# Performance work log

Hardware: AMD Instinct MI355X
Metric: run time of the kernel (lower is better)

Reference implementation:

```python
import jax, jax.numpy as jnp
import numpy as np

CHEB_K = 3
EMBED_DIM = 16
N_NODES = 2048
DIM = 64


def setup_inputs() -> dict:
    key = jax.random.key(0)
    k1, k2, k3, k4 = jax.random.split(key, 4)
    B, N, T, D = 16, N_NODES, 12, DIM
    x = jax.random.normal(k1, (B, N, T, D), dtype=jnp.float32)
    node_embeddings = jax.random.normal(k2, (N, EMBED_DIM), dtype=jnp.float32)
    # xavier-uniform-ish init for pools
    wp_bound = float(np.sqrt(6.0 / (EMBED_DIM * CHEB_K * D + D)))
    weights_pool = jax.random.uniform(k3, (EMBED_DIM, CHEB_K, D, D), dtype=jnp.float32,
                                      minval=-wp_bound, maxval=wp_bound)
    bias_pool = jax.random.uniform(k4, (EMBED_DIM, D), dtype=jnp.float32)
    return {"x": x, "node_embeddings": node_embeddings,
            "weights_pool": weights_pool, "bias_pool": bias_pool}


def reference(x, node_embeddings, weights_pool, bias_pool):
    B, N, T, D = x.shape
    cheb_k = weights_pool.shape[1]
    # [B,N,T,D] -> [B*T, N, D]
    xr = jnp.transpose(x, (0, 2, 1, 3)).reshape(B * T, N, D)
    # adaptive adjacency: row-softmax of relu gram matrix  [N,N]
    supports = jax.nn.softmax(jax.nn.relu(node_embeddings @ node_embeddings.T), axis=1)
    # Chebyshev polynomial basis of the adaptive support
    support_set = [jnp.eye(N, dtype=supports.dtype), supports]
    for _ in range(2, cheb_k):
        support_set.append(2.0 * supports @ support_set[-1] - support_set[-2])
    supports_k = jnp.stack(support_set, axis=0)  # [K,N,N]
    # hypernetwork: per-node weights/bias from embeddings
    weights = jnp.einsum('nd,dkio->nkio', node_embeddings, weights_pool)  # [N,K,D,D]
    bias = node_embeddings @ bias_pool  # [N,D]
    # graph conv: gather K-hop aggregates, then per-node grouped GEMM
    x_g = jnp.einsum('knm,bmc->bnkc', supports_k, xr)  # [B*T,N,K,D]
    x_gconv = jnp.einsum('bnki,nkio->bno', x_g, weights) + bias  # [B*T,N,D]
    return jnp.transpose(x_gconv.reshape(B, T, N, D), (0, 2, 1, 3))
```

## Files before the change

kernel.cpp:

```cpp
#include <hip/hip_runtime.h>
#include <hip/hip_bf16.h>

#define N_NODES 2048
#define EMB 16
#define NT 12
#define BT 192
#define C_COLS 12288
#define TD 768
#define BSTRIDE (N_NODES * TD)
#define KDIM 2048

typedef unsigned short u16;
typedef unsigned int u32;
typedef __attribute__((ext_vector_type(8))) __bf16 bf16x8;
typedef __attribute__((ext_vector_type(8))) u16 u16x8;
typedef __attribute__((ext_vector_type(4))) float f32x4;

__device__ __forceinline__ u16 f2bfu(float f) {
    u32 u = __float_as_uint(f);
    return (u16)((u + 0x7FFFu + ((u >> 16) & 1u)) >> 16);
}
__device__ __forceinline__ float bfu2f(u16 h) {
    return __uint_as_float(((u32)h) << 16);
}

__device__ __forceinline__ void gl2lds16(const void* g, void* l) {
    __builtin_amdgcn_global_load_lds(
        (const __attribute__((address_space(1))) u32*)g,
        (__attribute__((address_space(3))) u32*)l, 16, 0, 0);
}

__global__ void supports_kernel(const float* __restrict__ E, u16* __restrict__ Sb)
{
    __shared__ float en[EMB];
    __shared__ float red[256];
    const int n = blockIdx.x;
    const int tid = threadIdx.x;
    if (tid < EMB) en[tid] = E[n * EMB + tid];
    __syncthreads();

    float v[8];
    float mx = 0.0f;
    #pragma unroll
    for (int j = 0; j < 8; ++j) {
        const int m = tid + j * 256;
        const float* em = E + m * EMB;
        float acc = 0.f;
        #pragma unroll
        for (int d = 0; d < EMB; ++d) acc += en[d] * em[d];
        acc = fmaxf(acc, 0.f);
        v[j] = acc;
        mx = fmaxf(mx, acc);
    }
    red[tid] = mx;
    __syncthreads();
    for (int s = 128; s > 0; s >>= 1) {
        if (tid < s) red[tid] = fmaxf(red[tid], red[tid + s]);
        __syncthreads();
    }
    mx = red[0];
    __syncthreads();

    float sum = 0.f;
    #pragma unroll
    for (int j = 0; j < 8; ++j) { v[j] = __expf(v[j] - mx); sum += v[j]; }
    red[tid] = sum;
    __syncthreads();
    for (int s = 128; s > 0; s >>= 1) {
        if (tid < s) red[tid] += red[tid + s];
        __syncthreads();
    }
    const float inv = 1.f / red[0];
    #pragma unroll
    for (int j = 0; j < 8; ++j)
        Sb[(size_t)n * KDIM + tid + j * 256] = f2bfu(v[j] * inv);
}

__global__ void xcast_kernel(const float* __restrict__ x, u16* __restrict__ XbT, int c0g)
{
    __shared__ u16 tile[64][65];
    const int tid = threadIdx.x;
    const int cg = c0g + blockIdx.x * 64;
    const int b = cg / TD;
    const int r0 = cg - b * TD;
    const int m0 = blockIdx.y * 64;
    const float* xp = x + (size_t)b * BSTRIDE + (size_t)m0 * TD + r0;

    const int lc = tid & 63;
    const int rg = tid >> 6;
    #pragma unroll
    for (int j = 0; j < 16; ++j) {
        const int mr = j * 4 + rg;
        tile[lc][mr] = f2bfu(xp[(size_t)mr * TD + lc]);
    }
    __syncthreads();
    u16* op = XbT + (size_t)(blockIdx.x * 64) * KDIM + m0;
    #pragma unroll
    for (int j = 0; j < 16; ++j) {
        const int cr = j * 4 + rg;
        op[(size_t)cr * KDIM + lc] = tile[cr][lc];
    }
}

template <int MODE>
__launch_bounds__(256, 3)
__global__ void mfma_gemm(const u16* __restrict__ A,
                          const u16* __restrict__ B,
                          u16* __restrict__ OutT,
                          u16* __restrict__ OutRow,
                          const u16* __restrict__ Xc,
                          int c0g)
{
    __shared__ char smem[16384];
    char* As = smem;
    char* Bs = smem + 8192;

    const int tid = threadIdx.x;
    const int lane = tid & 63;
    const int w = tid >> 6;
    const int wm = w >> 1, wn = w & 1;
    const int ln15 = lane & 15, quad = lane >> 4;

    const int m0 = blockIdx.y * 128;
    const int cb = blockIdx.x * 128;

    const int q0 = 2 * w, q1 = 2 * w + 1;
    const int srow = lane >> 2;
    const int skol = (lane & 3) * 8;
    const u16* ga0 = A + (size_t)(m0 + q0 * 16 + srow) * KDIM + skol;
    const u16* ga1 = A + (size_t)(m0 + q1 * 16 + srow) * KDIM + skol;
    const u16* gb0 = B + (size_t)(cb + q0 * 16 + srow) * KDIM + skol;
    const u16* gb1 = B + (size_t)(cb + q1 * 16 + srow) * KDIM + skol;
    char* la0 = As + q0 * 1024;
    char* la1 = As + q1 * 1024;
    char* lb0 = Bs + q0 * 1024;
    char* lb1 = Bs + q1 * 1024;

    f32x4 acc[4][4] = {};

    for (int k0 = 0; k0 < KDIM; k0 += 32) {
        __syncthreads();
        gl2lds16(ga0, la0);
        gl2lds16(ga1, la1);
        gl2lds16(gb0, lb0);
        gl2lds16(gb1, lb1);
        ga0 += 32; ga1 += 32; gb0 += 32; gb1 += 32;
        __syncthreads();

        bf16x8 af[4], bg[4];
        #pragma unroll
        for (int i = 0; i < 4; ++i) {
            af[i] = *(const bf16x8*)(As + ((wm * 64 + i * 16 + ln15) * 64 + quad * 16));
            bg[i] = *(const bf16x8*)(Bs + ((wn * 64 + i * 16 + ln15) * 64 + quad * 16));
        }
        #pragma unroll
        for (int mi = 0; mi < 4; ++mi)
            #pragma unroll
            for (int ni = 0; ni < 4; ++ni)
                acc[mi][ni] = __builtin_amdgcn_mfma_f32_16x16x32_bf16(
                    af[mi], bg[ni], acc[mi][ni], 0, 0, 0);
    }

    const int mbase = m0 + wm * 64 + quad * 4;
    const int cbase = cb + wn * 64 + ln15;
    #pragma unroll
    for (int mi = 0; mi < 4; ++mi) {
        #pragma unroll
        for (int ni = 0; ni < 4; ++ni) {
            const f32x4 v = acc[mi][ni];
            const int mm = mbase + mi * 16;
            const int cc = cbase + ni * 16;
            if (MODE == 0) {
                ushort4 u;
                u.x = f2bfu(v.x); u.y = f2bfu(v.y); u.z = f2bfu(v.z); u.w = f2bfu(v.w);
                *(ushort4*)(OutT + (size_t)cc * KDIM + mm) = u;
                u16* orow = OutRow + (size_t)mm * C_COLS + c0g + cc;
                orow[0 * C_COLS] = u.x;
                orow[1 * C_COLS] = u.y;
                orow[2 * C_COLS] = u.z;
                orow[3 * C_COLS] = u.w;
            } else {
                const ushort4 xv = *(const ushort4*)(Xc + (size_t)cc * KDIM + mm);
                u16* orow = OutRow + (size_t)mm * C_COLS + c0g + cc;
                orow[0 * C_COLS] = f2bfu(2.f * v.x - bfu2f(xv.x));
                orow[1 * C_COLS] = f2bfu(2.f * v.y - bfu2f(xv.y));
                orow[2 * C_COLS] = f2bfu(2.f * v.z - bfu2f(xv.z));
                orow[3 * C_COLS] = f2bfu(2.f * v.w - bfu2f(xv.w));
            }
        }
    }
}

__launch_bounds__(256, 2)
__global__ void whyper_kernel(const float* __restrict__ E,
                              const float* __restrict__ Wp,
                              u16* __restrict__ Wrow)
{
    __shared__ float Es[32][16];
    const int tid = threadIdx.x;
    const int kt = blockIdx.x;
    const int n0 = blockIdx.y * 32;
    for (int i = tid; i < 512; i += 256)
        Es[i >> 4][i & 15] = E[(n0 + (i >> 4)) * EMB + (i & 15)];
    __syncthreads();

    const int o = tid & 63;
    const int kq = tid >> 6;
    #pragma unroll 1
    for (int it = 0; it < 6; ++it) {
        const int ki = kt * 24 + it * 4 + kq;
        const float* wp = Wp + (size_t)ki * 64 + o;
        float wv[EMB];
        #pragma unroll
        for (int d = 0; d < EMB; ++d) wv[d] = wp[(size_t)d * 12288];
        #pragma unroll 4
        for (int nn = 0; nn < 32; ++nn) {
            float a = 0.f;
            #pragma unroll
            for (int d = 0; d < EMB; ++d) a = fmaf(Es[nn][d], wv[d], a);
            Wrow[(size_t)(n0 + nn) * 12288 + (size_t)ki * 64 + o] = f2bfu(a);
        }
    }
}

__launch_bounds__(256, 2)
__global__ void wtrans_kernel(u16* __restrict__ Wbuf)
{
    __shared__ u16 Wt[64 * 192];
    const int n = blockIdx.x;
    const int tid = threadIdx.x;
    u16* Wn = Wbuf + (size_t)n * 12288;

    ushort4 va[6][2];
    #pragma unroll
    for (int j = 0; j < 6; ++j) {
        const int c = tid + j * 256;
        va[j][0] = *(const ushort4*)(Wn + c * 8);
        va[j][1] = *(const ushort4*)(Wn + c * 8 + 4);
    }
    #pragma unroll
    for (int j = 0; j < 6; ++j) {
        const int c = tid + j * 256;
        const int ki = c >> 3;
        const int o0 = (c & 7) * 8;
        Wt[(o0 + 0) * 192 + ki] = va[j][0].x;
        Wt[(o0 + 1) * 192 + ki] = va[j][0].y;
        Wt[(o0 + 2) * 192 + ki] = va[j][0].z;
        Wt[(o0 + 3) * 192 + ki] = va[j][0].w;
        Wt[(o0 + 4) * 192 + ki] = va[j][1].x;
        Wt[(o0 + 5) * 192 + ki] = va[j][1].y;
        Wt[(o0 + 6) * 192 + ki] = va[j][1].z;
        Wt[(o0 + 7) * 192 + ki] = va[j][1].w;
    }
    __syncthreads();

    #pragma unroll
    for (int j = 0; j < 6; ++j) {
        const int c = tid + j * 256;
        const int o = c / 24;
        const int kc = c - o * 24;
        const int ki0 = kc * 8;
        const int m = (o & 7) << 4;
        const ushort4 lo = *(const ushort4*)(Wt + o * 192 + ki0);
        const ushort4 hi = *(const ushort4*)(Wt + o * 192 + ki0 + 4);
        char* gp = (char*)Wbuf + (size_t)n * 24576 + o * 384 + ((ki0 * 2) ^ m);
        *(ushort4*)gp = lo;
        *(ushort4*)(gp + 8) = hi;
    }
}

__launch_bounds__(256, 4)
__global__ void gconv_mfma2_kernel(const float* __restrict__ x,
                                   const float* __restrict__ E,
                                   const float* __restrict__ Bp,
                                   const u16* __restrict__ Wall,
                                   const u16* __restrict__ Y1,
                                   const u16* __restrict__ Y2,
                                   float* __restrict__ Out)
{
    __shared__ char WsB[24576];
    __shared__ float en[EMB];
    __shared__ float bias[64];

    const int n = blockIdx.x;
    const int tid = threadIdx.x;
    const int lane = tid & 63;
    const int w = tid >> 6;

    if (tid < EMB) en[tid] = E[n * EMB + tid];

    const char* Wn = (const char*)Wall + (size_t)n * 24576;
    for (int iss = w; iss < 24; iss += 4)
        gl2lds16(Wn + iss * 1024 + lane * 16, WsB + iss * 1024);

    __syncthreads();

    if (tid < 64) {
        float a = 0.f;
        #pragma unroll
        for (int d = 0; d < EMB; ++d) a = fmaf(en[d], Bp[d * 64 + tid], a);
        bias[tid] = a;
    }
    __syncthreads();

    const int ln15 = lane & 15, quad = lane >> 4;
    const int q16 = quad * 16;
    const int m0w = w * 48;

    int rowb[4], msk[4];
    #pragma unroll
    for (int ni = 0; ni < 4; ++ni) {
        const int o = ni * 16 + ln15;
        rowb[ni] = o * 384;
        msk[ni] = (o & 7) << 4;
    }

    const float* xb[3];
    size_t yo[3];
    #pragma unroll
    for (int mi = 0; mi < 3; ++mi) {
        const int bt = m0w + mi * 16 + ln15;
        const int b = bt / NT, t = bt - b * NT;
        xb[mi] = x + (size_t)b * BSTRIDE + (size_t)n * TD + (size_t)t * 64 + quad * 8;
        yo[mi] = (size_t)n * C_COLS + (size_t)bt * 64 + quad * 8;
    }

    f32x4 acc[3][4] = {};

    #pragma unroll
    for (int ks = 0; ks < 2; ++ks) {
        bf16x8 af[3];
        #pragma unroll
        for (int mi = 0; mi < 3; ++mi) {
            const float* p = xb[mi] + ks * 32;
            const f32x4 lo = *(const f32x4*)p;
            const f32x4 hi = *(const f32x4*)(p + 4);
            u16x8 u;
            u[0] = f2bfu(lo.x); u[1] = f2bfu(lo.y); u[2] = f2bfu(lo.z); u[3] = f2bfu(lo.w);
            u[4] = f2bfu(hi.x); u[5] = f2bfu(hi.y); u[6] = f2bfu(hi.z); u[7] = f2bfu(hi.w);
            af[mi] = *(const bf16x8*)&u;
        }
        bf16x8 bg[4];
        #pragma unroll
        for (int ni = 0; ni < 4; ++ni)
            bg[ni] = *(const bf16x8*)(WsB + rowb[ni] + ((ks * 64 + q16) ^ msk[ni]));
        #pragma unroll
        for (int mi = 0; mi < 3; ++mi)
            #pragma unroll
            for (int ni = 0; ni < 4; ++ni)
                acc[mi][ni] = __builtin_amdgcn_mfma_f32_16x16x32_bf16(
                    af[mi], bg[ni], acc[mi][ni], 0, 0, 0);
    }

    const u16* ybase[2] = { Y1, Y2 };
    #pragma unroll
    for (int s = 0; s < 2; ++s) {
        const u16* Yb = ybase[s];
        #pragma unroll
        for (int ks = 0; ks < 2; ++ks) {
            bf16x8 af[3];
            #pragma unroll
            for (int mi = 0; mi < 3; ++mi)
                af[mi] = *(const bf16x8*)(Yb + yo[mi] + ks * 32);
            bf16x8 bg[4];
            #pragma unroll
            for (int ni = 0; ni < 4; ++ni)
                bg[ni] = *(const bf16x8*)(WsB + rowb[ni] + 128 + s * 128
                                          + ((ks * 64 + q16) ^ msk[ni]));
            #pragma unroll
            for (int mi = 0; mi < 3; ++mi)
                #pragma unroll
                for (int ni = 0; ni < 4; ++ni)
                    acc[mi][ni] = __builtin_amdgcn_mfma_f32_16x16x32_bf16(
                        af[mi], bg[ni], acc[mi][ni], 0, 0, 0);
        }
    }

    float bv[4];
    #pragma unroll
    for (int ni = 0; ni < 4; ++ni) bv[ni] = bias[ni * 16 + ln15];

    #pragma unroll
    for (int mi = 0; mi < 3; ++mi) {
        const int rowb2 = m0w + mi * 16 + quad * 4;
        #pragma unroll
        for (int r = 0; r < 4; ++r) {
            const int bt = rowb2 + r;
            const int b = bt / NT, t = bt - b * NT;
            float* op = Out + (((size_t)(b * N_NODES + n)) * NT + t) * 64 + ln15;
            #pragma unroll
            for (int ni = 0; ni < 4; ++ni)
                op[ni * 16] = acc[mi][ni][r] + bv[ni];
        }
    }
}

__launch_bounds__(256, 4)
__global__ void gconv_mfma_kernel(const float* __restrict__ x,
                                  const float* __restrict__ E,
                                  const float* __restrict__ Wp,
                                  const float* __restrict__ Bp,
                                  const u16* __restrict__ Y1,
                                  const u16* __restrict__ Y2,
                                  float* __restrict__ Out)
{
    __shared__ u16 Ws[64][200];
    __shared__ float en[EMB];
    __shared__ float bias[64];

    const int n = blockIdx.x;
    const int tid = threadIdx.x;
    if (tid < EMB) en[tid] = E[n * EMB + tid];
    __syncthreads();

    {
        const int o = tid & 63;
        const int kio = tid >> 6;
        #pragma unroll 4
        for (int j = 0; j < 48; ++j) {
            const int ki = j * 4 + kio;
            const float* wp = Wp + ki * 64 + o;
            float a = 0.f;
            #pragma unroll
            for (int d = 0; d < EMB; ++d) a = fmaf(en[d], wp[d * 12288], a);
            Ws[o][ki] = f2bfu(a);
        }
        if (tid < 64) {
            float a = 0.f;
            #pragma unroll
            for (int d = 0; d < EMB; ++d) a = fmaf(en[d], Bp[d * 64 + tid], a);
            bias[tid] = a;
        }
    }
    __syncthreads();

    const int lane = tid & 63;
    const int w = tid >> 6;
    const int ln15 = lane & 15, quad = lane >> 4;
    const int m0w = w * 48;

    const float* xb[3];
    size_t yo[3];
    #pragma unroll
    for (int mi = 0; mi < 3; ++mi) {
        const int bt = m0w + mi * 16 + ln15;
        const int b = bt / NT, t = bt - b * NT;
        xb[mi] = x + (size_t)b * BSTRIDE + (size_t)n * TD + (size_t)t * 64 + quad * 8;
        yo[mi] = (size_t)n * C_COLS + (size_t)bt * 64 + quad * 8;
    }

    f32x4 acc[3][4] = {};

    #pragma unroll
    for (int ks = 0; ks < 2; ++ks) {
        bf16x8 af[3];
        #pragma unroll
        for (int mi = 0; mi < 3; ++mi) {
            const float* p = xb[mi] + ks * 32;
            const f32x4 lo = *(const f32x4*)p;
            const f32x4 hi = *(const f32x4*)(p + 4);
            u16x8 u;
            u[0] = f2bfu(lo.x); u[1] = f2bfu(lo.y); u[2] = f2bfu(lo.z); u[3] = f2bfu(lo.w);
            u[4] = f2bfu(hi.x); u[5] = f2bfu(hi.y); u[6] = f2bfu(hi.z); u[7] = f2bfu(hi.w);
            af[mi] = *(const bf16x8*)&u;
        }
        bf16x8 bg[4];
        #pragma unroll
        for (int ni = 0; ni < 4; ++ni)
            bg[ni] = *(const bf16x8*)&Ws[ni * 16 + ln15][ks * 32 + quad * 8];
        #pragma unroll
        for (int mi = 0; mi < 3; ++mi)
            #pragma unroll
            for (int ni = 0; ni < 4; ++ni)
                acc[mi][ni] = __builtin_amdgcn_mfma_f32_16x16x32_bf16(
                    af[mi], bg[ni], acc[mi][ni], 0, 0, 0);
    }

    const u16* ybase[2] = { Y1, Y2 };
    #pragma unroll
    for (int s = 0; s < 2; ++s) {
        const u16* Yb = ybase[s];
        #pragma unroll
        for (int ks = 0; ks < 2; ++ks) {
            bf16x8 af[3];
            #pragma unroll
            for (int mi = 0; mi < 3; ++mi)
                af[mi] = *(const bf16x8*)(Yb + yo[mi] + ks * 32);
            bf16x8 bg[4];
            #pragma unroll
            for (int ni = 0; ni < 4; ++ni)
                bg[ni] = *(const bf16x8*)&Ws[ni * 16 + ln15][64 + s * 64 + ks * 32 + quad * 8];
            #pragma unroll
            for (int mi = 0; mi < 3; ++mi)
                #pragma unroll
                for (int ni = 0; ni < 4; ++ni)
                    acc[mi][ni] = __builtin_amdgcn_mfma_f32_16x16x32_bf16(
                        af[mi], bg[ni], acc[mi][ni], 0, 0, 0);
        }
    }

    float bv[4];
    #pragma unroll
    for (int ni = 0; ni < 4; ++ni) bv[ni] = bias[ni * 16 + ln15];

    #pragma unroll
    for (int mi = 0; mi < 3; ++mi) {
        const int rowb = m0w + mi * 16 + quad * 4;
        #pragma unroll
        for (int r = 0; r < 4; ++r) {
            const int bt = rowb + r;
            const int b = bt / NT, t = bt - b * NT;
            float* op = Out + (((size_t)(b * N_NODES + n)) * NT + t) * 64 + ln15;
            #pragma unroll
            for (int ni = 0; ni < 4; ++ni)
                op[ni * 16] = acc[mi][ni][r] + bv[ni];
        }
    }
}

extern "C" void kernel_launch(void* const* d_in, const int* in_sizes, int n_in,
                              void* d_out, int out_size, void* d_ws, size_t ws_size,
                              hipStream_t stream)
{
    const float* x  = (const float*)d_in[0];
    const float* E  = (const float*)d_in[1];
    const float* Wp = (const float*)d_in[2];
    const float* Bp = (const float*)d_in[3];
    float* Out = (float*)d_out;

    const size_t MiB = 1024 * 1024;
    u16* Sb    = (u16*)d_ws;
    u16* Y1row = (u16*)((char*)d_ws + 8 * MiB);
    u16* Y2row = (u16*)((char*)d_ws + 56 * MiB);
    char* chunkbase = (char*)d_ws + 104 * MiB;

    size_t wall_off = 0;
    bool newpath = false;
    if (ws_size >= 160 * MiB) {
        wall_off = ((ws_size - 48 * MiB) / 256) * 256;
        if (wall_off >= 112 * MiB) newpath = true;
    }
    const size_t budget = newpath ? wall_off : ws_size;

    const int cands[5] = {1, 2, 3, 6, 12};
    int nc = 12;
    for (int i = 0; i < 5; ++i) {
        const size_t chunk_bytes = (size_t)(C_COLS / cands[i]) * KDIM * 2;
        if (104 * MiB + 2 * chunk_bytes <= budget) { nc = cands[i]; break; }
    }
    const int CW = C_COLS / nc;
    u16* XbTc = (u16*)chunkbase;
    u16* Y1Tc = (u16*)(chunkbase + (size_t)CW * KDIM * 2);
    u16* Wbuf = (u16*)((char*)d_ws + wall_off);

    supports_kernel<<<N_NODES, 256, 0, stream>>>(E, Sb);

    if (newpath) {
        whyper_kernel<<<dim3(8, 64), 256, 0, stream>>>(E, Wp, Wbuf);
        wtrans_kernel<<<N_NODES, 256, 0, stream>>>(Wbuf);
    }

    for (int c = 0; c < nc; ++c) {
        const int c0g = c * CW;
        xcast_kernel<<<dim3(CW / 64, 32), 256, 0, stream>>>(x, XbTc, c0g);
        mfma_gemm<0><<<dim3(CW / 128, 16), 256, 0, stream>>>(Sb, XbTc, Y1Tc, Y1row, nullptr, c0g);
        mfma_gemm<1><<<dim3(CW / 128, 16), 256, 0, stream>>>(Sb, Y1Tc, nullptr, Y2row, XbTc, c0g);
    }

    if (newpath)
        gconv_mfma2_kernel<<<N_NODES, 256, 0, stream>>>(x, E, Bp, Wbuf, Y1row, Y2row, Out);
    else
        gconv_mfma_kernel<<<N_NODES, 256, 0, stream>>>(x, E, Wp, Bp, Y1row, Y2row, Out);
}
```

Measured before the change: 578.3 us.

## Add 256x256 bf16 MFMA GEMM path with swizzled layouts and stacked A operand

When the workspace holds at least 216 MiB, a new path runs. It precomputes T2 = 2*S*S - I with a 256x256-tile MFMA GEMM, then computes both S·X and T2·X in one GEMM launch by treating Sb and T2b as one 4096-row A operand. The new GEMM uses 512-thread blocks, a 128 KiB double-buffered LDS pipeline fed by global_load_lds, and XOR-swizzled K layouts written by the producer kernels to avoid LDS bank conflicts. This is meant to raise MFMA utilisation and drop the chunked path. In exchange it adds an extra N^3 GEMM and a transpose, needs a larger workspace, and stays inactive if the harness provides less than 216 MiB.

```diff
diff --git a/kernel.cpp b/kernel.cpp
--- a/kernel.cpp
+++ b/kernel.cpp
@@ -30,6 +30,10 @@
         (__attribute__((address_space(3))) u32*)l, 16, 0, 0);
 }
 
+__device__ __forceinline__ int cswz(int col, int row) {
+    return (col & ~63) | ((((col >> 3) ^ row) & 7) << 3) | (col & 7);
+}
+
 __global__ void supports_kernel(const float* __restrict__ E, u16* __restrict__ Sb)
 {
     __shared__ float en[EMB];
@@ -74,6 +78,78 @@
     #pragma unroll
     for (int j = 0; j < 8; ++j)
         Sb[(size_t)n * KDIM + tid + j * 256] = f2bfu(v[j] * inv);
+}
+
+__global__ void supports2_kernel(const float* __restrict__ E, u16* __restrict__ Sb)
+{
+    __shared__ float en[EMB];
+    __shared__ float red[256];
+    const int n = blockIdx.x;
+    const int tid = threadIdx.x;
+    if (tid < EMB) en[tid] = E[n * EMB + tid];
+    __syncthreads();
+
+    float v[8];
+    float mx = 0.0f;
+    #pragma unroll
+    for (int j = 0; j < 8; ++j) {
+        const int m = tid + j * 256;
+        const float* em = E + m * EMB;
+        float acc = 0.f;
+        #pragma unroll
+        for (int d = 0; d < EMB; ++d) acc += en[d] * em[d];
+        acc = fmaxf(acc, 0.f);
+        v[j] = acc;
+        mx = fmaxf(mx, acc);
+    }
+    red[tid] = mx;
+    __syncthreads();
+    for (int s = 128; s > 0; s >>= 1) {
+        if (tid < s) red[tid] = fmaxf(red[tid], red[tid + s]);
+        __syncthreads();
+    }
+    mx = red[0];
+    __syncthreads();
+
+    float sum = 0.f;
+    #pragma unroll
+    for (int j = 0; j < 8; ++j) { v[j] = __expf(v[j] - mx); sum += v[j]; }
+    red[tid] = sum;
+    __syncthreads();
+    for (int s = 128; s > 0; s >>= 1) {
+        if (tid < s) red[tid] += red[tid + s];
+        __syncthreads();
+    }
+    const float inv = 1.f / red[0];
+    #pragma unroll
+    for (int j = 0; j < 8; ++j) {
+        const int m = tid + j * 256;
+        Sb[(size_t)n * KDIM + cswz(m, n)] = f2bfu(v[j] * inv);
+    }
+}
+
+__global__ void strans_kernel(const u16* __restrict__ Sb, u16* __restrict__ SbT)
+{
+    __shared__ u16 T[64][65];
+    const int tid = threadIdx.x;
+    const int n0 = blockIdx.y * 64;
+    const int j0 = blockIdx.x * 64;
+    const int lc = tid & 63;
+    const int rg = tid >> 6;
+    #pragma unroll
+    for (int j = 0; j < 16; ++j) {
+        const int r = j * 4 + rg;
+        const u16 vv = Sb[(size_t)(n0 + r) * KDIM + j0 + lc];
+        const int jt = ((((lc >> 3) ^ (n0 + r)) & 7) << 3) | (lc & 7);
+        T[jt][r] = vv;
+    }
+    __syncthreads();
+    #pragma unroll
+    for (int j = 0; j < 16; ++j) {
+        const int jj = j * 4 + rg;
+        const int cs = ((((lc >> 3) ^ (j0 + jj)) & 7) << 3) | (lc & 7);
+        SbT[(size_t)(j0 + jj) * KDIM + n0 + cs] = T[jj][lc];
+    }
 }
 
 __global__ void xcast_kernel(const float* __restrict__ x, u16* __restrict__ XbT, int c0g)
@@ -99,6 +175,148 @@
     for (int j = 0; j < 16; ++j) {
         const int cr = j * 4 + rg;
         op[(size_t)cr * KDIM + lc] = tile[cr][lc];
+    }
+}
+
+__global__ void xcast2_kernel(const float* __restrict__ x, u16* __restrict__ XbT)
+{
+    __shared__ u16 tile[64][65];
+    const int tid = threadIdx.x;
+    const int cg = blockIdx.x * 64;
+    const int b = cg / TD;
+    const int r0 = cg - b * TD;
+    const int m0 = blockIdx.y * 64;
+    const float* xp = x + (size_t)b * BSTRIDE + (size_t)m0 * TD + r0;
+
+    const int lc = tid & 63;
+    const int rg = tid >> 6;
+    #pragma unroll
+    for (int j = 0; j < 16; ++j) {
+        const int mr = j * 4 + rg;
+        tile[lc][mr] = f2bfu(xp[(size_t)mr * TD + lc]);
+    }
+    __syncthreads();
+    u16* op = XbT + (size_t)cg * KDIM + m0;
+    #pragma unroll
+    for (int j = 0; j < 16; ++j) {
+        const int cr = j * 4 + rg;
+        const int ls = ((((lc >> 3) ^ cr) & 7) << 3) | (lc & 7);
+        op[(size_t)cr * KDIM + ls] = tile[cr][lc];
+    }
+}
+
+template <int MODE>
+__launch_bounds__(512, 2)
+__global__ void gemm256(const u16* __restrict__ A, const u16* __restrict__ B,
+                        u16* __restrict__ O1, u16* __restrict__ O2)
+{
+    __shared__ char smem[131072];
+    const int tid = threadIdx.x;
+    const int lane = tid & 63;
+    const int w = tid >> 6;
+    const int wm = w >> 2, wn = w & 3;
+    const int ln15 = lane & 15, quad = lane >> 4;
+
+    const int m0 = blockIdx.y * 256;
+    const int c0 = blockIdx.x * 256;
+
+    const int srow = lane >> 3;
+    const int sbyte = (lane & 7) * 16;
+    const char* gA = (const char*)A + (size_t)(m0 + w * 32 + srow) * 4096 + sbyte;
+    const char* gB = (const char*)B + (size_t)(c0 + w * 32 + srow) * 4096 + sbyte;
+    char* lA = smem + w * 4096;
+    char* lB = smem + 32768 + w * 4096;
+
+    auto stage = [&](int t, int buf) {
+        #pragma unroll
+        for (int j = 0; j < 4; ++j) {
+            gl2lds16(gA + (size_t)j * 32768 + (size_t)t * 128,
+                     lA + buf * 65536 + j * 1024);
+            gl2lds16(gB + (size_t)j * 32768 + (size_t)t * 128,
+                     lB + buf * 65536 + j * 1024);
+        }
+    };
+
+    stage(0, 0);
+    stage(1, 1);
+    asm volatile("s_waitcnt vmcnt(8)" ::: "memory");
+    __builtin_amdgcn_sched_barrier(0);
+    __builtin_amdgcn_s_barrier();
+
+    f32x4 acc[8][4] = {};
+    const int arow0 = wm * 128 + ln15;
+    const int brow0 = wn * 64 + ln15;
+    const int xorm = (ln15 & 7) << 4;
+
+    const int NTI = KDIM / 64;
+    #pragma unroll 1
+    for (int t = 0; t < NTI; ++t) {
+        const char* Ab = smem + (t & 1) * 65536;
+        const char* Bb = Ab + 32768;
+        #pragma unroll
+        for (int kh = 0; kh < 2; ++kh) {
+            const int koff = (kh * 64 + quad * 16) ^ xorm;
+            bf16x8 af[8], bg[4];
+            #pragma unroll
+            for (int mi = 0; mi < 8; ++mi)
+                af[mi] = *(const bf16x8*)(Ab + (arow0 + mi * 16) * 128 + koff);
+            #pragma unroll
+            for (int ni = 0; ni < 4; ++ni)
+                bg[ni] = *(const bf16x8*)(Bb + (brow0 + ni * 16) * 128 + koff);
+            #pragma unroll
+            for (int mi = 0; mi < 8; ++mi)
+                #pragma unroll
+                for (int ni = 0; ni < 4; ++ni)
+                    acc[mi][ni] = __builtin_amdgcn_mfma_f32_16x16x32_bf16(
+                        af[mi], bg[ni], acc[mi][ni], 0, 0, 0);
+        }
+        __builtin_amdgcn_sched_barrier(0);
+        __builtin_amdgcn_s_barrier();
+        __builtin_amdgcn_sched_barrier(0);
+        if (t + 2 < NTI) {
+            stage(t + 2, t & 1);
+            asm volatile("s_waitcnt vmcnt(8)" ::: "memory");
+        } else {
+            asm volatile("s_waitcnt vmcnt(0)" ::: "memory");
+        }
+        __builtin_amdgcn_sched_barrier(0);
+        __builtin_amdgcn_s_barrier();
+        __builtin_amdgcn_sched_barrier(0);
+    }
+
+    const int mbase = m0 + wm * 128 + quad * 4;
+    const int cbase = c0 + wn * 64 + ln15;
+    if (MODE == 0) {
+        #pragma unroll
+        for (int mi = 0; mi < 8; ++mi) {
+            #pragma unroll
+            for (int ni = 0; ni < 4; ++ni) {
+                const f32x4 v = acc[mi][ni];
+                const int cc = cbase + ni * 16;
+                #pragma unroll
+                for (int r = 0; r < 4; ++r) {
+                    const int mm = mbase + mi * 16 + r;
+                    const float t2 = 2.f * v[r] - ((mm == cc) ? 1.f : 0.f);
+                    O1[(size_t)mm * KDIM + cswz(cc, mm)] = f2bfu(t2);
+                }
+            }
+        }
+    } else {
+        u16* Ob = (m0 < 2048) ? O1 : O2;
+        const int mb = (m0 < 2048) ? mbase : (mbase - 2048);
+        #pragma unroll
+        for (int mi = 0; mi < 8; ++mi) {
+            #pragma unroll
+            for (int ni = 0; ni < 4; ++ni) {
+                const f32x4 v = acc[mi][ni];
+                const int cc = cbase + ni * 16;
+                u16* orow = Ob + (size_t)(mb + mi * 16) * C_COLS + cc;
+                orow[0 * C_COLS] = f2bfu(v.x);
+                orow[1 * C_COLS] = f2bfu(v.y);
+                orow[2 * C_COLS] = f2bfu(v.z);
+                orow[3 * C_COLS] = f2bfu(v.w);
+            }
+        }
     }
 }
 
@@ -529,6 +747,28 @@
     float* Out = (float*)d_out;
 
     const size_t MiB = 1024 * 1024;
+
+    if (ws_size >= 216 * MiB) {
+        u16* Sb    = (u16*)d_ws;
+        u16* T2b   = (u16*)((char*)d_ws + 8 * MiB);
+        u16* SbT   = (u16*)((char*)d_ws + 16 * MiB);
+        u16* Y1row = (u16*)((char*)d_ws + 24 * MiB);
+        u16* Y2row = (u16*)((char*)d_ws + 72 * MiB);
+        u16* XbT   = (u16*)((char*)d_ws + 120 * MiB);
+        u16* Wbuf  = (u16*)((char*)d_ws + 168 * MiB);
+
+        supports2_kernel<<<N_NODES, 256, 0, stream>>>(E, Sb);
+        strans_kernel<<<dim3(32, 32), 256, 0, stream>>>(Sb, SbT);
+        gemm256<0><<<dim3(8, 8), 512, 0, stream>>>(Sb, SbT, T2b, nullptr);
+        xcast2_kernel<<<dim3(192, 32), 256, 0, stream>>>(x, XbT);
+        gemm256<1><<<dim3(48, 16), 512, 0, stream>>>(Sb, XbT, Y1row, Y2row);
+
+        whyper_kernel<<<dim3(8, 64), 256, 0, stream>>>(E, Wp, Wbuf);
+        wtrans_kernel<<<N_NODES, 256, 0, stream>>>(Wbuf);
+        gconv_mfma2_kernel<<<N_NODES, 256, 0, stream>>>(x, E, Bp, Wbuf, Y1row, Y2row, Out);
+        return;
+    }
+
     u16* Sb    = (u16*)d_ws;
     u16* Y1row = (u16*)((char*)d_ws + 8 * MiB);
     u16* Y2row = (u16*)((char*)d_ws + 56 * MiB);
```

Result: faster. 548.0 us (-5.3%).
